# Optimization experiments

Hardware: AMD Instinct MI355X
Metric: run time of the kernel (lower is better)

The kernel has to match this reference:

```python
import jax, jax.numpy as jnp
import numpy as np

B, T, D = 4, 2048, 1024
H, DK, DV = 16, 64, 64
SCALE = 1.0 / np.sqrt(DK).astype(np.float32)
DROPOUT_P = 0.5  # torch F.dropout default


def setup_inputs() -> dict:
    key = jax.random.key(0)
    ks = jax.random.split(key, 12)
    s = 0.02
    x = jax.random.normal(ks[0], (B, T, D), jnp.float32)
    # additive causal mask: 0 on/below diagonal, -1e9 above
    causal = jnp.where(jnp.tril(jnp.ones((T, T), jnp.bool_)), 0.0, -1e9).astype(jnp.float32)
    attn_mask = causal[None, None, :, :]
    Wq = jax.random.normal(ks[1], (H, D, DK), jnp.float32) * s
    bq = jax.random.normal(ks[2], (H, DK), jnp.float32) * s
    Wk = jax.random.normal(ks[3], (H, D, DK), jnp.float32) * s
    bk = jax.random.normal(ks[4], (H, DK), jnp.float32) * s
    Wv = jax.random.normal(ks[5], (H, D, DV), jnp.float32) * s
    bv = jax.random.normal(ks[6], (H, DV), jnp.float32) * s
    Wout = jax.random.normal(ks[7], (D, D), jnp.float32) * s
    bout = jax.random.normal(ks[8], (D,), jnp.float32) * s
    keep = jax.random.bernoulli(ks[9], 1.0 - DROPOUT_P, (B, T, D))
    dropout_mask = keep.astype(jnp.float32) / (1.0 - DROPOUT_P)
    return {"x": x, "attn_mask": attn_mask, "Wq": Wq, "bq": bq, "Wk": Wk,
            "bk": bk, "Wv": Wv, "bv": bv, "Wout": Wout, "bout": bout,
            "dropout_mask": dropout_mask}


def reference(x, attn_mask, Wq, bq, Wk, bk, Wv, bv, Wout, bout, dropout_mask):
    # batched per-head projections (equivalent to the per-head nn.Linear loop)
    Q = jnp.einsum('btd,hdk->bhtk', x, Wq) + bq[None, :, None, :]
    K = jnp.einsum('btd,hdk->bhtk', x, Wk) + bk[None, :, None, :]
    V = jnp.einsum('btd,hdv->bhtv', x, Wv) + bv[None, :, None, :]
    # scaled dot-product attention
    scores = jnp.einsum('bhqk,bhmk->bhqm', Q, K) * SCALE + attn_mask
    attn = jax.nn.softmax(scores, axis=-1)
    ctx = jnp.einsum('bhqm,bhmv->bhqv', attn, V)          # [B,H,T,DV]
    # faithful to original: view without transposing heads/time
    ctx = ctx.reshape(B, T, H * DV)
    out = ctx @ Wout.T + bout
    out = out * dropout_mask                               # deterministic dropout
    return out
```

## Files before the change

### kernel.cpp

```cpp
#include <hip/hip_runtime.h>
#include <stdint.h>
#include <stddef.h>

typedef short s8v __attribute__((ext_vector_type(8)));
typedef float f4  __attribute__((ext_vector_type(4)));
typedef float f16v __attribute__((ext_vector_type(16)));
typedef unsigned int u32;
typedef unsigned int u32x2 __attribute__((ext_vector_type(2)));
typedef unsigned int u32x4 __attribute__((ext_vector_type(4)));

#define SCALE2_ 0.18033688011112042f
#define NEG_BIG -3.0e38f
#define AS1 __attribute__((address_space(1)))
#define AS3 __attribute__((address_space(3)))

static __device__ __forceinline__ short f2bf(float f) {
    u32 u = __builtin_bit_cast(u32, f);
    u = (u + 0x7fffu + ((u >> 16) & 1u)) >> 16;
    return (short)u;
}

static __device__ __forceinline__ u32 cvtpk(float lo, float hi) {
    u32 r;
    asm("v_cvt_pk_bf16_f32 %0, %1, %2" : "=v"(r) : "v"(lo), "v"(hi));
    return r;
}

static __device__ __forceinline__ float hexp2(float x) {
    float r;
    asm("v_exp_f32 %0, %1" : "=v"(r) : "v"(x));
    return r;
}


__global__ __launch_bounds__(256) void k_prep(
    const float* __restrict__ x,    s8v* __restrict__ xb,
    const float* __restrict__ wout, s8v* __restrict__ woutb,
    const float* __restrict__ Wq, const float* __restrict__ Wk,
    const float* __restrict__ Wv,   s8v* __restrict__ wqkvb,
    const float* __restrict__ bq, const float* __restrict__ bk,
    const float* __restrict__ bv,   float* __restrict__ bqkv)
{
    int i = blockIdx.x * 256 + threadIdx.x;
    if (i < 1048576 + 131072) {
        const float* src = (i < 1048576) ? x : wout;
        s8v* dst = (i < 1048576) ? xb : woutb;
        const int k = (i < 1048576) ? i : (i - 1048576);
        const float4* p = (const float4*)src;
        float4 a = p[2 * k], b = p[2 * k + 1];
        s8v o;
        o[0] = f2bf(a.x); o[1] = f2bf(a.y); o[2] = f2bf(a.z); o[3] = f2bf(a.w);
        o[4] = f2bf(b.x); o[5] = f2bf(b.y); o[6] = f2bf(b.z); o[7] = f2bf(b.w);
        dst[k] = o;
        return;
    }
    i -= 1048576 + 131072;
    if (i < 393216) {
        const int n = i >> 7, d8 = i & 127;
        const float* W = (n < 1024) ? Wq : ((n < 2048) ? Wk : Wv);
        const float sc = (n < 1024) ? SCALE2_ : 1.0f;
        const int nn = n & 1023;
        const float* src = W + (size_t)((nn >> 6) * 1024 + d8 * 8) * 64 + (nn & 63);
        s8v o;
        #pragma unroll
        for (int k = 0; k < 8; k++) o[k] = f2bf(src[k * 64] * sc);
        wqkvb[i] = o;
        return;
    }
    i -= 393216;
    if (i < 3072) {
        const float* b = (i < 1024) ? bq : ((i < 2048) ? bk : bv);
        bqkv[i] = b[i & 1023] * ((i < 1024) ? SCALE2_ : 1.0f);
    }
}


template <int EPI, int KDIM>
__global__ __launch_bounds__(256) void gemm128(
    const short* __restrict__ A, const short* __restrict__ Bt,
    int M, int N,
    const float* __restrict__ bias,
    const float* __restrict__ drop, float* __restrict__ outf,
    short* __restrict__ outq, short* __restrict__ outk, short* __restrict__ outv)
{
    __shared__ __align__(16) short lA[128 * 64];
    __shared__ __align__(16) short lB[128 * 64];
    const int tid = threadIdx.x;
    const int w = tid >> 6, l = tid & 63;
    const int wm = w >> 1, wn = w & 1;
    const int lr = l & 15, lg = l >> 4;
    const int lr3 = l >> 3, cg = (l & 7) ^ lr3;
    const int bm = blockIdx.y * 128, bn = blockIdx.x * 128;
    constexpr int NT = KDIM >> 6;

    const short* Abl = A + ((size_t)bm + lr3) * KDIM + cg * 8;
    const short* Bbl = Bt + ((size_t)bn + lr3) * KDIM + cg * 8;

    f4 acc[4][4] = {};

    #pragma unroll 1
    for (int kt = 0; kt < NT; kt++) {
        if (kt) __syncthreads();
        #pragma unroll
        for (int i = 0; i < 4; i++) {
            const int rg = w * 32 + i * 8;
            __builtin_amdgcn_global_load_lds(
                (const AS1 void*)(Abl + (size_t)rg * KDIM + kt * 64),
                (AS3 void*)(lA + rg * 64), 16, 0, 0);
            __builtin_amdgcn_global_load_lds(
                (const AS1 void*)(Bbl + (size_t)rg * KDIM + kt * 64),
                (AS3 void*)(lB + rg * 64), 16, 0, 0);
        }
        __syncthreads();
        #pragma unroll
        for (int c = 0; c < 2; c++) {
            s8v af[4], bfv[4];
            #pragma unroll
            for (int mt = 0; mt < 4; mt++)
                af[mt] = *(const s8v*)&lA[(wm * 64 + mt * 16 + lr) * 64
                                          + (((c * 4 + lg) ^ (lr & 7)) << 3)];
            #pragma unroll
            for (int nt = 0; nt < 4; nt++)
                bfv[nt] = *(const s8v*)&lB[(wn * 64 + nt * 16 + lr) * 64
                                           + (((c * 4 + lg) ^ (lr & 7)) << 3)];
            __builtin_amdgcn_s_setprio(1);
            #pragma unroll
            for (int mt = 0; mt < 4; mt++)
                #pragma unroll
                for (int nt = 0; nt < 4; nt++)
                    acc[mt][nt] = __builtin_amdgcn_mfma_f32_16x16x32_bf16(
                        af[mt], bfv[nt], acc[mt][nt], 0, 0, 0);
            __builtin_amdgcn_s_setprio(0);
        }
    }

    if (EPI == 0) {
        const int pq = bm >> 10;
        #pragma unroll
        for (int mt = 0; mt < 4; mt++) {
            const int m0 = bm + wm * 64 + mt * 16 + lg * 4;
            const float4 bb = *(const float4*)&bias[m0];
            const int hh = (m0 >> 6) & 15, kk0 = m0 & 63;
            #pragma unroll
            for (int nt = 0; nt < 4; nt++) {
                const int n = bn + wn * 64 + nt * 16 + lr;
                const int b = n >> 11, t = n & 2047;
                const size_t bh = (size_t)(b * 16 + hh);
                const float v0 = acc[mt][nt][0] + bb.x, v1 = acc[mt][nt][1] + bb.y;
                const float v2 = acc[mt][nt][2] + bb.z, v3 = acc[mt][nt][3] + bb.w;
                if (pq == 2) {
                    short* d = outv + bh * 131072 + (size_t)kk0 * 2048 + t;
                    d[0] = f2bf(v0); d[2048] = f2bf(v1);
                    d[4096] = f2bf(v2); d[6144] = f2bf(v3);
                } else {
                    short* d = ((pq == 0) ? outq : outk) + (bh * 2048 + t) * 64 + kk0;
                    u32x2 pr = {cvtpk(v0, v1), cvtpk(v2, v3)};
                    *(u32x2*)d = pr;
                }
            }
        }
    } else {
        #pragma unroll
        for (int mt = 0; mt < 4; mt++) {
            const int m0 = bm + wm * 64 + mt * 16 + lg * 4;
            #pragma unroll
            for (int nt = 0; nt < 4; nt++) {
                const int n = bn + wn * 64 + nt * 16 + lr;
                const float bb = bias[n];
                #pragma unroll
                for (int j = 0; j < 4; j++) {
                    const size_t off = (size_t)(m0 + j) * N + n;
                    outf[off] = (acc[mt][nt][j] + bb) * drop[off];
                }
            }
        }
    }
}


__global__ __launch_bounds__(256, 4) void attn_fwd(
    const short* __restrict__ Q, const short* __restrict__ Kv,
    const short* __restrict__ Vt, short* __restrict__ Ctx)
{
    const int i = blockIdx.x;
    const int bh = (i & 7) * 8 + ((i >> 3) & 7);
    const int g = (i >> 6) & 3, rr = i >> 8;
    const int qb = (rr == 0) ? (15 - g) : (rr == 1) ? g : (rr == 2) ? (11 - g) : (4 + g);
    const int tid = threadIdx.x, w = tid >> 6, l = tid & 63;
    const int lq = l & 31, hh = l >> 5;

    __shared__ short smem[16384];

    const size_t base = (size_t)bh * 131072;
    const short* Kg = Kv + base;
    const short* Vg = Vt + base;

    auto stage = [&](int j) {
        short* kb = smem + (j & 1) * 4096;
        short* vb = smem + 8192 + (j & 1) * 4096;
        const int cg = (l & 7) ^ (l >> 3);
        #pragma unroll
        for (int i2 = 0; i2 < 2; i2++) {
            const int r2 = w * 16 + i2 * 8 + (l >> 3);
            __builtin_amdgcn_global_load_lds(
                (const AS1 void*)(Kg + (size_t)(j * 64 + r2) * 64 + cg * 8),
                (AS3 void*)(kb + (w * 16 + i2 * 8) * 64), 16, 0, 0);
            __builtin_amdgcn_global_load_lds(
                (const AS1 void*)(Vg + (size_t)r2 * 2048 + j * 64 + cg * 8),
                (AS3 void*)(vb + (w * 16 + i2 * 8) * 64), 16, 0, 0);
        }
    };

    const int nj = 2 * qb + 2;
    const int qt0 = qb * 128 + w * 32;
    const int qrow = qt0 + lq;

    s8v qf[4];
    #pragma unroll
    for (int m = 0; m < 4; m++)
        qf[m] = *(const s8v*)&Q[base + (size_t)(qt0 + lq) * 64 + m * 16 + hh * 8];

    f16v acc0 = {}, acc1 = {};
    float l_run = 0.f;

    stage(0);

    for (int j = 0; j < nj; j++) {
        __syncthreads();
        const short* kb = smem + (j & 1) * 4096;
        const short* vb = smem + 8192 + (j & 1) * 4096;
        if (j + 1 < nj) stage(j + 1);

        if (64 * j > qt0 + 31) continue;

        f16v sA = {}, sB = {};
        #pragma unroll
        for (int m = 0; m < 4; m++) {
            const int ck = ((2 * m + hh) ^ (l & 7)) * 8;
            const s8v ka = *(const s8v*)&kb[lq * 64 + ck];
            const s8v kc = *(const s8v*)&kb[(32 + lq) * 64 + ck];
            sA = __builtin_amdgcn_mfma_f32_32x32x16_bf16(ka, qf[m], sA, 0, 0, 0);
            sB = __builtin_amdgcn_mfma_f32_32x32x16_bf16(kc, qf[m], sB, 0, 0, 0);
        }

        if (64 * j + 63 > qt0) {
            #pragma unroll
            for (int r = 0; r < 16; r++) {
                const int klo = 64 * j + (r & 3) + 8 * (r >> 2) + 4 * hh;
                if (klo > qrow)      sA[r] = NEG_BIG;
                if (klo + 32 > qrow) sB[r] = NEG_BIG;
            }
        }

        #pragma unroll
        for (int r = 0; r < 16; r++) {
            sA[r] = hexp2(sA[r]);
            sB[r] = hexp2(sB[r]);
        }
        float sm[8];
        #pragma unroll
        for (int r = 0; r < 8; r++)
            sm[r] = (sA[r] + sA[r + 8]) + (sB[r] + sB[r + 8]);
        l_run += ((sm[0] + sm[1]) + (sm[2] + sm[3])) +
                 ((sm[4] + sm[5]) + (sm[6] + sm[7]));

        #pragma unroll
        for (int m = 0; m < 4; m++) {
            const int rb = (m & 1) * 8;
            u32 P0, P1, P2, P3;
            if (m < 2) {
                P0 = cvtpk(sA[rb + 0], sA[rb + 1]); P1 = cvtpk(sA[rb + 2], sA[rb + 3]);
                P2 = cvtpk(sA[rb + 4], sA[rb + 5]); P3 = cvtpk(sA[rb + 6], sA[rb + 7]);
            } else {
                P0 = cvtpk(sB[rb + 0], sB[rb + 1]); P1 = cvtpk(sB[rb + 2], sB[rb + 3]);
                P2 = cvtpk(sB[rb + 4], sB[rb + 5]); P3 = cvtpk(sB[rb + 6], sB[rb + 7]);
            }
            const u32x2 s02 = __builtin_amdgcn_permlane32_swap(P0, P2, false, false);
            const u32x2 s13 = __builtin_amdgcn_permlane32_swap(P1, P3, false, false);
            const u32x4 uv = {s02[0], s13[0], s02[1], s13[1]};
            const s8v pf = __builtin_bit_cast(s8v, uv);

            const int ck = ((2 * m + hh) ^ (l & 7)) * 8;
            const s8v va = *(const s8v*)&vb[lq * 64 + ck];
            const s8v vc = *(const s8v*)&vb[(32 + lq) * 64 + ck];
            acc0 = __builtin_amdgcn_mfma_f32_32x32x16_bf16(va, pf, acc0, 0, 0, 0);
            acc1 = __builtin_amdgcn_mfma_f32_32x32x16_bf16(vc, pf, acc1, 0, 0, 0);
        }
    }

    __syncthreads();
    {
        const float lt = l_run + __shfl_xor(l_run, 32);
        const float inv = 1.f / lt;
        short* Os = smem + w * 2176;
        #pragma unroll
        for (int r = 0; r < 16; r += 2) {
            const int v0 = (r & 3) + 8 * (r >> 2) + 4 * hh;
            *(u32*)&Os[lq * 68 + v0]      = cvtpk(acc0[r] * inv, acc0[r + 1] * inv);
            *(u32*)&Os[lq * 68 + 32 + v0] = cvtpk(acc1[r] * inv, acc1[r + 1] * inv);
        }
        #pragma unroll
        for (int c = 0; c < 4; c++) {
            const s8v o = *(const s8v*)&Os[(l >> 1) * 68 + (l & 1) * 32 + c * 8];
            *(s8v*)&Ctx[base + (size_t)(qt0 + (l >> 1)) * 64 + (l & 1) * 32 + c * 8] = o;
        }
    }
}


#define WS_XB   ((size_t)0)
#define WS_WQKV ((size_t)16777216)
#define WS_WOUT ((size_t)23068672)
#define WS_BQKV ((size_t)25165824)
#define WS_Q    ((size_t)25178112)
#define WS_K    ((size_t)41955328)
#define WS_V    ((size_t)58732544)
#define WS_CTX  ((size_t)75509760)

extern "C" void kernel_launch(void* const* d_in, const int* in_sizes, int n_in,
                              void* d_out, int out_size, void* d_ws, size_t ws_size,
                              hipStream_t stream) {
    const float* x    = (const float*)d_in[0];
    const float* Wq   = (const float*)d_in[2];
    const float* bq   = (const float*)d_in[3];
    const float* Wk   = (const float*)d_in[4];
    const float* bk   = (const float*)d_in[5];
    const float* Wv   = (const float*)d_in[6];
    const float* bv   = (const float*)d_in[7];
    const float* Wout = (const float*)d_in[8];
    const float* bout = (const float*)d_in[9];
    const float* drop = (const float*)d_in[10];
    float* out = (float*)d_out;

    char* ws = (char*)d_ws;
    short* Xb    = (short*)(ws + WS_XB);
    short* Wqkvb = (short*)(ws + WS_WQKV);
    short* Woutb = (short*)(ws + WS_WOUT);
    float* bqkv  = (float*)(ws + WS_BQKV);
    short* Qb    = (short*)(ws + WS_Q);
    short* Kb    = (short*)(ws + WS_K);
    short* Vtb   = (short*)(ws + WS_V);
    short* Ctxb  = (short*)(ws + WS_CTX);

    k_prep<<<6156, 256, 0, stream>>>(x, (s8v*)Xb, Wout, (s8v*)Woutb,
                                     Wq, Wk, Wv, (s8v*)Wqkvb,
                                     bq, bk, bv, bqkv);

    gemm128<0, 1024><<<dim3(64, 24), 256, 0, stream>>>(
        Wqkvb, Xb, 3072, 8192, bqkv, nullptr, nullptr, Qb, Kb, Vtb);

    attn_fwd<<<dim3(1024), 256, 0, stream>>>(Qb, Kb, Vtb, Ctxb);

    gemm128<1, 1024><<<dim3(8, 64), 256, 0, stream>>>(
        Ctxb, Woutb, 8192, 1024, bout, drop, out, nullptr, nullptr, nullptr);
}
```

Baseline: 165.9 us.

## Triple-buffer K tiles and split K/V prefetch with fine-grained vmcnt waits

The attention kernel's single double-buffered K+V stage is split into separate K and V loads. K is now triple-buffered and prefetched two tiles ahead, V is prefetched one tile ahead, and the full __syncthreads is replaced by an explicit vmcnt wait plus s_barrier. MFMA sections are wrapped in s_setprio to favour matrix work over other waves. The aim is to hide global-to-LDS latency for K. In exchange, LDS use grows from 32 KB to 40 KB per block, which may limit occupancy, and the hand-counted vmcnt is fragile.

```diff
diff --git a/kernel.cpp b/kernel.cpp
--- a/kernel.cpp
+++ b/kernel.cpp
@@ -189,24 +189,30 @@
     const int tid = threadIdx.x, w = tid >> 6, l = tid & 63;
     const int lq = l & 31, hh = l >> 5;
 
-    __shared__ short smem[16384];
+    __shared__ short smem[20480];
 
     const size_t base = (size_t)bh * 131072;
     const short* Kg = Kv + base;
     const short* Vg = Vt + base;
-
-    auto stage = [&](int j) {
-        short* kb = smem + (j & 1) * 4096;
-        short* vb = smem + 8192 + (j & 1) * 4096;
-        const int cg = (l & 7) ^ (l >> 3);
+    const int cgs = (l & 7) ^ (l >> 3);
+
+    auto stageK = [&](int j, int s) {
+        short* kb = smem + s * 4096;
         #pragma unroll
         for (int i2 = 0; i2 < 2; i2++) {
             const int r2 = w * 16 + i2 * 8 + (l >> 3);
             __builtin_amdgcn_global_load_lds(
-                (const AS1 void*)(Kg + (size_t)(j * 64 + r2) * 64 + cg * 8),
+                (const AS1 void*)(Kg + (size_t)(j * 64 + r2) * 64 + cgs * 8),
                 (AS3 void*)(kb + (w * 16 + i2 * 8) * 64), 16, 0, 0);
+        }
+    };
+    auto stageV = [&](int j, int s) {
+        short* vb = smem + 12288 + s * 4096;
+        #pragma unroll
+        for (int i2 = 0; i2 < 2; i2++) {
+            const int r2 = w * 16 + i2 * 8 + (l >> 3);
             __builtin_amdgcn_global_load_lds(
-                (const AS1 void*)(Vg + (size_t)r2 * 2048 + j * 64 + cg * 8),
+                (const AS1 void*)(Vg + (size_t)r2 * 2048 + j * 64 + cgs * 8),
                 (AS3 void*)(vb + (w * 16 + i2 * 8) * 64), 16, 0, 0);
         }
     };
@@ -223,17 +229,35 @@
     f16v acc0 = {}, acc1 = {};
     float l_run = 0.f;
 
-    stage(0);
-
+    __builtin_amdgcn_sched_barrier(0);
+    stageK(0, 0);
+    stageV(0, 0);
+    if (1 < nj) stageK(1, 1);
+    __builtin_amdgcn_sched_barrier(0);
+
+    int ks = 0;
+    int kss = 2;
+
+    #pragma unroll 1
     for (int j = 0; j < nj; j++) {
-        __syncthreads();
-        const short* kb = smem + (j & 1) * 4096;
-        const short* vb = smem + 8192 + (j & 1) * 4096;
-        if (j + 1 < nj) stage(j + 1);
+        if (j + 1 < nj) asm volatile("s_waitcnt vmcnt(2)" ::: "memory");
+        else            asm volatile("s_waitcnt vmcnt(0)" ::: "memory");
+        __builtin_amdgcn_s_barrier();
+        __builtin_amdgcn_sched_barrier(0);
+
+        if (j + 1 < nj) stageV(j + 1, (j & 1) ^ 1);
+        if (j + 2 < nj) stageK(j + 2, kss);
+        __builtin_amdgcn_sched_barrier(0);
+
+        const short* kb = smem + ks * 4096;
+        const short* vb = smem + 12288 + (j & 1) * 4096;
+        ks = (ks == 2) ? 0 : ks + 1;
+        kss = (kss == 2) ? 0 : kss + 1;
 
         if (64 * j > qt0 + 31) continue;
 
         f16v sA = {}, sB = {};
+        __builtin_amdgcn_s_setprio(1);
         #pragma unroll
         for (int m = 0; m < 4; m++) {
             const int ck = ((2 * m + hh) ^ (l & 7)) * 8;
@@ -242,6 +266,7 @@
             sA = __builtin_amdgcn_mfma_f32_32x32x16_bf16(ka, qf[m], sA, 0, 0, 0);
             sB = __builtin_amdgcn_mfma_f32_32x32x16_bf16(kc, qf[m], sB, 0, 0, 0);
         }
+        __builtin_amdgcn_s_setprio(0);
 
         if (64 * j + 63 > qt0) {
             #pragma unroll
@@ -264,6 +289,7 @@
         l_run += ((sm[0] + sm[1]) + (sm[2] + sm[3])) +
                  ((sm[4] + sm[5]) + (sm[6] + sm[7]));
 
+        __builtin_amdgcn_s_setprio(1);
         #pragma unroll
         for (int m = 0; m < 4; m++) {
             const int rb = (m & 1) * 8;
@@ -286,6 +312,7 @@
             acc0 = __builtin_amdgcn_mfma_f32_32x32x16_bf16(va, pf, acc0, 0, 0, 0);
             acc1 = __builtin_amdgcn_mfma_f32_32x32x16_bf16(vc, pf, acc1, 0, 0, 0);
         }
+        __builtin_amdgcn_s_setprio(0);
     }
 
     __syncthreads();
```

Result: slower. 170.0 us (+2.4%).

## Replace QKV projection GEMM with 8-wave 256x128 triple-buffered pipelined kernel

Applied to the files above, without the earlier changes.

Adds a new GEMM kernel with 512 threads computing 256x128 output tiles. It stages data through a three-stage LDS ring via direct global-to-LDS loads, interleaving prefetch of later K tiles with MFMA phases and raising wave priority during the math. The QKV projection launch now uses it in place of the 128x128 kernel, aiming to hide global load latency and reuse each B tile across more rows. The cost is a large LDS footprint (about 144 KB) that limits occupancy, plus many barriers per K step.

```diff
diff --git a/kernel.cpp b/kernel.cpp
--- a/kernel.cpp
+++ b/kernel.cpp
@@ -76,6 +76,183 @@
 
 
 template <int EPI, int KDIM>
+__global__ __launch_bounds__(512, 2) void gemm8p(
+    const short* __restrict__ A, const short* __restrict__ Bt,
+    int M, int N,
+    const float* __restrict__ bias,
+    const float* __restrict__ drop, float* __restrict__ outf,
+    short* __restrict__ outq, short* __restrict__ outk, short* __restrict__ outv)
+{
+    __shared__ __align__(16) short lds[73728];
+    const int tid = threadIdx.x;
+    const int w = tid >> 6, l = tid & 63;
+    const int wm = w >> 1, wn = w & 1;
+    const int lr = l & 15, lg = l >> 4;
+    const int lr3 = l >> 3, cg = (l & 7) ^ lr3;
+    const int bm = blockIdx.y * 256, bn = blockIdx.x * 128;
+    constexpr int NT = KDIM >> 6;
+
+    const short* Abl = A + ((size_t)bm + lr3) * KDIM + cg * 8;
+    const short* Bbl = Bt + ((size_t)bn + lr3) * KDIM + cg * 8;
+
+    auto STAGE_A = [&](int kt, int s, int half) {
+        short* la = lds + s * 16384;
+        #pragma unroll
+        for (int i = half * 2; i < half * 2 + 2; i++) {
+            const int rg = i * 64 + w * 8;
+            __builtin_amdgcn_global_load_lds(
+                (const AS1 void*)(Abl + (size_t)rg * KDIM + kt * 64),
+                (AS3 void*)(la + rg * 64), 16, 0, 0);
+        }
+    };
+    auto STAGE_B = [&](int kt, int s) {
+        short* lb = lds + 49152 + s * 8192;
+        #pragma unroll
+        for (int i = 0; i < 2; i++) {
+            const int rg = i * 64 + w * 8;
+            __builtin_amdgcn_global_load_lds(
+                (const AS1 void*)(Bbl + (size_t)rg * KDIM + kt * 64),
+                (AS3 void*)(lb + rg * 64), 16, 0, 0);
+        }
+    };
+
+    f4 acc[4][4] = {};
+
+    STAGE_A(0, 0, 0); STAGE_A(0, 0, 1); STAGE_B(0, 0);
+    STAGE_A(1, 1, 0); STAGE_A(1, 1, 1); STAGE_B(1, 1);
+    asm volatile("s_waitcnt vmcnt(6)" ::: "memory");
+    __builtin_amdgcn_s_barrier();
+    __builtin_amdgcn_sched_barrier(0);
+
+    int sr = 0;
+    #pragma unroll 1
+    for (int kt = 0; kt < NT; kt++) {
+        const int sn = (sr == 0) ? 2 : sr - 1;
+        const bool pf = (kt + 2 < NT);
+        const short* sa = lds + sr * 16384;
+        const short* sb = lds + 49152 + sr * 8192;
+        const int off0 = (lg ^ (lr & 7)) << 3;
+        const int off1 = ((4 + lg) ^ (lr & 7)) << 3;
+
+        s8v af[4], b0, b1;
+
+        #pragma unroll
+        for (int mt = 0; mt < 4; mt++)
+            af[mt] = *(const s8v*)&sa[(wm * 64 + mt * 16 + lr) * 64 + off0];
+        b0 = *(const s8v*)&sb[(wn * 64 + lr) * 64 + off0];
+        b1 = *(const s8v*)&sb[(wn * 64 + 16 + lr) * 64 + off0];
+        if (pf) STAGE_A(kt + 2, sn, 0);
+        __builtin_amdgcn_s_barrier();
+        asm volatile("s_waitcnt lgkmcnt(0)" ::: "memory");
+        __builtin_amdgcn_sched_barrier(0);
+        __builtin_amdgcn_s_setprio(1);
+        #pragma unroll
+        for (int mt = 0; mt < 4; mt++) {
+            acc[mt][0] = __builtin_amdgcn_mfma_f32_16x16x32_bf16(af[mt], b0, acc[mt][0], 0, 0, 0);
+            acc[mt][1] = __builtin_amdgcn_mfma_f32_16x16x32_bf16(af[mt], b1, acc[mt][1], 0, 0, 0);
+        }
+        __builtin_amdgcn_s_setprio(0);
+        __builtin_amdgcn_s_barrier();
+
+        b0 = *(const s8v*)&sb[(wn * 64 + 32 + lr) * 64 + off0];
+        b1 = *(const s8v*)&sb[(wn * 64 + 48 + lr) * 64 + off0];
+        if (pf) STAGE_A(kt + 2, sn, 1);
+        __builtin_amdgcn_s_barrier();
+        asm volatile("s_waitcnt lgkmcnt(0)" ::: "memory");
+        __builtin_amdgcn_sched_barrier(0);
+        __builtin_amdgcn_s_setprio(1);
+        #pragma unroll
+        for (int mt = 0; mt < 4; mt++) {
+            acc[mt][2] = __builtin_amdgcn_mfma_f32_16x16x32_bf16(af[mt], b0, acc[mt][2], 0, 0, 0);
+            acc[mt][3] = __builtin_amdgcn_mfma_f32_16x16x32_bf16(af[mt], b1, acc[mt][3], 0, 0, 0);
+        }
+        __builtin_amdgcn_s_setprio(0);
+        __builtin_amdgcn_s_barrier();
+
+        #pragma unroll
+        for (int mt = 0; mt < 4; mt++)
+            af[mt] = *(const s8v*)&sa[(wm * 64 + mt * 16 + lr) * 64 + off1];
+        b0 = *(const s8v*)&sb[(wn * 64 + lr) * 64 + off1];
+        b1 = *(const s8v*)&sb[(wn * 64 + 16 + lr) * 64 + off1];
+        if (pf) STAGE_B(kt + 2, sn);
+        __builtin_amdgcn_s_barrier();
+        asm volatile("s_waitcnt lgkmcnt(0)" ::: "memory");
+        __builtin_amdgcn_sched_barrier(0);
+        __builtin_amdgcn_s_setprio(1);
+        #pragma unroll
+        for (int mt = 0; mt < 4; mt++) {
+            acc[mt][0] = __builtin_amdgcn_mfma_f32_16x16x32_bf16(af[mt], b0, acc[mt][0], 0, 0, 0);
+            acc[mt][1] = __builtin_amdgcn_mfma_f32_16x16x32_bf16(af[mt], b1, acc[mt][1], 0, 0, 0);
+        }
+        __builtin_amdgcn_s_setprio(0);
+        __builtin_amdgcn_s_barrier();
+
+        b0 = *(const s8v*)&sb[(wn * 64 + 32 + lr) * 64 + off1];
+        b1 = *(const s8v*)&sb[(wn * 64 + 48 + lr) * 64 + off1];
+        __builtin_amdgcn_s_barrier();
+        asm volatile("s_waitcnt lgkmcnt(0)" ::: "memory");
+        __builtin_amdgcn_sched_barrier(0);
+        __builtin_amdgcn_s_setprio(1);
+        #pragma unroll
+        for (int mt = 0; mt < 4; mt++) {
+            acc[mt][2] = __builtin_amdgcn_mfma_f32_16x16x32_bf16(af[mt], b0, acc[mt][2], 0, 0, 0);
+            acc[mt][3] = __builtin_amdgcn_mfma_f32_16x16x32_bf16(af[mt], b1, acc[mt][3], 0, 0, 0);
+        }
+        __builtin_amdgcn_s_setprio(0);
+        if (kt < NT - 1) {
+            if (pf) asm volatile("s_waitcnt vmcnt(6)" ::: "memory");
+            else    asm volatile("s_waitcnt vmcnt(0)" ::: "memory");
+            __builtin_amdgcn_s_barrier();
+            __builtin_amdgcn_sched_barrier(0);
+        }
+        sr = (sr == 2) ? 0 : sr + 1;
+    }
+
+    if (EPI == 0) {
+        const int pq = bm >> 10;
+        #pragma unroll
+        for (int mt = 0; mt < 4; mt++) {
+            const int m0 = bm + wm * 64 + mt * 16 + lg * 4;
+            const float4 bb = *(const float4*)&bias[m0];
+            const int hh = (m0 >> 6) & 15, kk0 = m0 & 63;
+            #pragma unroll
+            for (int nt = 0; nt < 4; nt++) {
+                const int n = bn + wn * 64 + nt * 16 + lr;
+                const int b = n >> 11, t = n & 2047;
+                const size_t bh = (size_t)(b * 16 + hh);
+                const float v0 = acc[mt][nt][0] + bb.x, v1 = acc[mt][nt][1] + bb.y;
+                const float v2 = acc[mt][nt][2] + bb.z, v3 = acc[mt][nt][3] + bb.w;
+                if (pq == 2) {
+                    short* d = outv + bh * 131072 + (size_t)kk0 * 2048 + t;
+                    d[0] = f2bf(v0); d[2048] = f2bf(v1);
+                    d[4096] = f2bf(v2); d[6144] = f2bf(v3);
+                } else {
+                    short* d = ((pq == 0) ? outq : outk) + (bh * 2048 + t) * 64 + kk0;
+                    u32x2 pr = {cvtpk(v0, v1), cvtpk(v2, v3)};
+                    *(u32x2*)d = pr;
+                }
+            }
+        }
+    } else {
+        #pragma unroll
+        for (int mt = 0; mt < 4; mt++) {
+            const int m0 = bm + wm * 64 + mt * 16 + lg * 4;
+            #pragma unroll
+            for (int nt = 0; nt < 4; nt++) {
+                const int n = bn + wn * 64 + nt * 16 + lr;
+                const float bb = bias[n];
+                #pragma unroll
+                for (int j = 0; j < 4; j++) {
+                    const size_t off = (size_t)(m0 + j) * N + n;
+                    outf[off] = (acc[mt][nt][j] + bb) * drop[off];
+                }
+            }
+        }
+    }
+}
+
+
+template <int EPI, int KDIM>
 __global__ __launch_bounds__(256) void gemm128(
     const short* __restrict__ A, const short* __restrict__ Bt,
     int M, int N,
@@ -346,7 +523,7 @@
                                      Wq, Wk, Wv, (s8v*)Wqkvb,
                                      bq, bk, bv, bqkv);
 
-    gemm128<0, 1024><<<dim3(64, 24), 256, 0, stream>>>(
+    gemm8p<0, 1024><<<dim3(64, 12), 512, 0, stream>>>(
         Wqkvb, Xb, 3072, 8192, bqkv, nullptr, nullptr, Qb, Kb, Vtb);
 
     attn_fwd<<<dim3(1024), 256, 0, stream>>>(Qb, Kb, Vtb, Ctxb);
```

Result: slower. 174.9 us (+5.4%).
